# Kernel tuning notes

Hardware: AMD Instinct MI355X
Metric: run time of the kernel (lower is better)

## Reference

```python
import jax, jax.numpy as jnp
import numpy as np

BN_EPS = 1e-5


def setup_inputs() -> dict:
    key = jax.random.key(0)
    ks = jax.random.split(key, 6)
    B, C, H, W = 4, 256, 64, 64
    Ci = 128
    s_in = 0.02  # small init scale for conv weights
    x = jax.random.normal(ks[0], (B, C, H, W), dtype=jnp.float32)
    g_w = jax.random.normal(ks[1], (Ci, C), dtype=jnp.float32) * s_in
    theta_w = jax.random.normal(ks[2], (Ci, C), dtype=jnp.float32) * s_in
    phi_w = jax.random.normal(ks[3], (Ci, C), dtype=jnp.float32) * s_in
    W_w = jax.random.normal(ks[4], (C, Ci), dtype=jnp.float32) * s_in
    return {
        "x": x,
        "g_w": g_w, "g_b": jnp.zeros((Ci,), jnp.float32),
        "theta_w": theta_w, "theta_b": jnp.zeros((Ci,), jnp.float32),
        "phi_w": phi_w, "phi_b": jnp.zeros((Ci,), jnp.float32),
        "W_w": W_w, "W_b": jnp.zeros((C,), jnp.float32),
        "bn_gamma": jnp.ones((C,), jnp.float32),
        "bn_beta": jnp.zeros((C,), jnp.float32),
    }


def reference(x, g_w, g_b, theta_w, theta_b, phi_w, phi_b, W_w, W_b, bn_gamma, bn_beta):
    B, C, H, W = x.shape
    N = H * W
    xf = x.reshape(B, C, N)  # flatten spatial -> [B, C, N]

    def conv1x1(w, b):  # 1x1 conv == per-position linear over channels
        return jnp.einsum('oc,bcn->bon', w, xf) + b[None, :, None]

    g_x = conv1x1(g_w, g_b)          # [B, Ci, N]
    theta_x = conv1x1(theta_w, theta_b)
    phi_x = conv1x1(phi_w, phi_b)

    f = jnp.einsum('bcn,bcm->bnm', theta_x, phi_x)   # [B, N, N] attention logits
    attn = jax.nn.softmax(f, axis=-1)
    y = jnp.einsum('bnm,bcm->bcn', attn, g_x)        # [B, Ci, N]

    Wy = jnp.einsum('oc,bcn->bon', W_w, y) + W_b[None, :, None]  # [B, C, N]
    Wy = Wy.reshape(B, C, H, W)

    # BatchNorm2d in training mode (default): batch statistics over (B, H, W)
    mean = Wy.mean(axis=(0, 2, 3))
    var = Wy.var(axis=(0, 2, 3))
    Wy_bn = (bn_gamma[None, :, None, None] * (Wy - mean[None, :, None, None])
             * jax.lax.rsqrt(var[None, :, None, None] + BN_EPS)
             + bn_beta[None, :, None, None])
    return Wy_bn + x
```

## Files before the change

kernel.cpp:

```cpp
#include <hip/hip_runtime.h>
#include <hip/hip_bf16.h>

typedef __attribute__((ext_vector_type(8))) __bf16 bf16x8;
typedef __attribute__((ext_vector_type(4))) __bf16 bf16x4;
typedef __attribute__((ext_vector_type(4))) float  f32x4;
typedef __attribute__((ext_vector_type(16))) float f32x16;

#define L2E 1.44269504088896340736f

static __device__ __forceinline__ f32x4 mfma16(bf16x8 a, bf16x8 b, f32x4 c) {
    return __builtin_amdgcn_mfma_f32_16x16x32_bf16(a, b, c, 0, 0, 0);
}
static __device__ __forceinline__ f32x16 mfma32(bf16x8 a, bf16x8 b, f32x16 c) {
    return __builtin_amdgcn_mfma_f32_32x32x16_bf16(a, b, c, 0, 0, 0);
}

#define GLOAD_LDS16(gsrc, ldst)                                                \
    __builtin_amdgcn_global_load_lds(                                          \
        (const __attribute__((address_space(1))) unsigned int*)(gsrc),         \
        (__attribute__((address_space(3))) unsigned int*)(ldst), 16, 0, 0)

__global__ __launch_bounds__(256) void prep_w(
    const float* __restrict__ thw, const float* __restrict__ phw,
    const float* __restrict__ gw,  const float* __restrict__ Ww,
    __bf16* __restrict__ wbf)
{
    const int idx  = blockIdx.x * 256 + threadIdx.x;
    const int base = idx * 4;
    const float* src = (base < 32768) ? thw : (base < 65536) ? phw
                     : (base < 98304) ? gw  : Ww;
    const int off = base & 32767;
    f32x4 v = *reinterpret_cast<const f32x4*>(src + off);
    bf16x4 o;
    #pragma unroll
    for (int i = 0; i < 4; ++i) o[i] = (__bf16)v[i];
    *reinterpret_cast<bf16x4*>(wbf + base) = o;
}

__global__ __launch_bounds__(256) void xT_kernel(
    const float* __restrict__ x, __bf16* __restrict__ xT)
{
    __shared__ float tile[64][65];
    const int b  = blockIdx.z;
    const int c0 = blockIdx.y * 64;
    const int n0 = blockIdx.x * 64;
    const int tr = threadIdx.x >> 4;
    const int tc = threadIdx.x & 15;
    #pragma unroll
    for (int k = 0; k < 4; ++k) {
        int c = k * 16 + tr;
        f32x4 v = *reinterpret_cast<const f32x4*>(
            x + ((size_t)b * 256 + c0 + c) * 4096 + n0 + tc * 4);
        #pragma unroll
        for (int i = 0; i < 4; ++i) tile[c][tc * 4 + i] = v[i];
    }
    __syncthreads();
    #pragma unroll
    for (int k = 0; k < 4; ++k) {
        int n = k * 16 + tr;
        bf16x4 v;
        #pragma unroll
        for (int i = 0; i < 4; ++i) v[i] = (__bf16)tile[tc * 4 + i][n];
        *reinterpret_cast<bf16x4*>(xT + ((size_t)b * 4096 + n0 + n) * 256 + c0 + tc * 4) = v;
    }
}

__global__ __launch_bounds__(256, 1) void proj_mfma(
    const __bf16* __restrict__ xT, const __bf16* __restrict__ wbf,
    const float* __restrict__ bth, const float* __restrict__ bph,
    const float* __restrict__ bg,
    __bf16* __restrict__ thetaT, __bf16* __restrict__ phiT, __bf16* __restrict__ gBlk)
{
    const int p    = blockIdx.y;
    const int b    = blockIdx.z;
    const int n0   = blockIdx.x * 64;
    const int w    = threadIdx.x >> 6;
    const int lane = threadIdx.x & 63;
    const int lo   = lane & 15;
    const int hi   = lane >> 4;

    __shared__ alignas(16) __bf16 XA[64 * 256];
    __shared__ alignas(16) __bf16 WL[128 * 256];

    const __bf16* wsrc  = wbf + p * 32768;
    const float*  bias  = (p == 0) ? bth : (p == 1) ? bph : bg;
    const __bf16* xbase = xT + ((size_t)b * 4096 + n0) * 256;

    #pragma unroll
    for (int u = 0; u < 8; ++u) {
        const int chunk = (w * 8 + u) * 64 + lane;
        const int row   = chunk >> 5;
        const int jb    = (chunk & 31) * 16;
        const int sb    = row * 512 + (jb ^ ((row & 7) << 4));
        GLOAD_LDS16(xbase + (sb >> 1), &XA[(w * 8 + u) * 512]);
    }
    #pragma unroll
    for (int u = 0; u < 16; ++u) {
        const int chunk = (w * 16 + u) * 64 + lane;
        const int row   = chunk >> 5;
        const int jb    = (chunk & 31) * 16;
        const int sb    = row * 512 + (jb ^ ((row & 7) << 4));
        GLOAD_LDS16(wsrc + (sb >> 1), &WL[(w * 16 + u) * 512]);
    }
    __syncthreads();

    f32x4 C[8];
    #pragma unroll
    for (int cc = 0; cc < 8; ++cc) C[cc] = f32x4{0.f, 0.f, 0.f, 0.f};

    const int arow = w * 16 + lo;
    #pragma unroll
    for (int kb = 0; kb < 8; ++kb) {
        const int koff = kb * 64 + hi * 16;
        bf16x8 a = *reinterpret_cast<const bf16x8*>(
            (const char*)XA + arow * 512 + (koff ^ ((arow & 7) << 4)));
        bf16x8 bb[8];
        #pragma unroll
        for (int cc = 0; cc < 8; ++cc) {
            const int o = cc * 16 + lo;
            bb[cc] = *reinterpret_cast<const bf16x8*>(
                (const char*)WL + o * 512 + (koff ^ ((o & 7) << 4)));
        }
        #pragma unroll
        for (int cc = 0; cc < 8; ++cc) C[cc] = mfma16(a, bb[cc], C[cc]);
    }

    if (p < 2) {
        __bf16* out = (p == 0) ? thetaT : phiT;
        const int nbase = n0 + w * 16;
        #pragma unroll
        for (int cc = 0; cc < 8; ++cc) {
            const float bv = bias[cc * 16 + lo];
            #pragma unroll
            for (int r = 0; r < 4; ++r)
                out[((size_t)b * 4096 + nbase + 4 * hi + r) * 128 + cc * 16 + lo] =
                    (__bf16)(C[cc][r] + bv);
        }
    } else {
        __syncthreads();
        __bf16* T = &XA[0];
        const int nl0 = w * 16 + 4 * hi;
        #pragma unroll
        for (int cc = 0; cc < 8; ++cc) {
            const float bv = bias[cc * 16 + lo];
            #pragma unroll
            for (int r = 0; r < 4; ++r)
                T[(cc * 16 + lo) * 66 + nl0 + r] = (__bf16)(C[cc][r] + bv);
        }
        __syncthreads();
        #pragma unroll
        for (int q8 = 0; q8 < 8; ++q8) {
            const int qid = q8 * 256 + threadIdx.x;
            const int c   = qid >> 4;
            const int nl  = (qid & 15) * 4;
            const int n   = n0 + nl;
            const int mt  = n >> 5;
            const int mm  = n & 31;
            const int g   = mm >> 2;
            const int gp  = (g & 4) | ((g & 1) << 1) | ((g >> 1) & 1);
            bf16x4 v;
            #pragma unroll
            for (int i = 0; i < 4; ++i) v[i] = T[c * 66 + nl + i];
            *reinterpret_cast<bf16x4*>(
                gBlk + (((size_t)(b * 128 + mt)) * 128 + c) * 32 + (gp << 2)) = v;
        }
    }
}

template<int NCH>
__global__ __launch_bounds__(256, 3) void attn_kernel(
    const __bf16* __restrict__ thetaT, const __bf16* __restrict__ phiT,
    const __bf16* __restrict__ gBlk, __bf16* __restrict__ yPart,
    float* __restrict__ lPart)
{
    constexpr int SH = (NCH == 8) ? 3 : 2;
    constexpr int NT = (4096 / NCH) / 32;
    const int bid   = blockIdx.x;
    const int chunk = bid & (NCH - 1);
    const int qb    = (bid >> SH) & 31;
    const int b     = bid >> (SH + 5);
    const int w     = threadIdx.x >> 6;
    const int lane  = threadIdx.x & 63;
    const int l31   = lane & 31;
    const int h2    = lane >> 5;
    const int Q0    = qb * 128 + w * 32;
    const int kvbase = chunk * (4096 / NCH);

    __shared__ alignas(16) __bf16 Kt[3][32 * 128];
    __shared__ alignas(16) __bf16 Vt[3][128 * 32];

    bf16x8 qf[8];
    {
        const __bf16* qrow = thetaT + ((size_t)b * 4096 + Q0 + l31) * 128 + h2 * 8;
        #pragma unroll
        for (int ks = 0; ks < 8; ++ks)
            qf[ks] = *reinterpret_cast<const bf16x8*>(qrow + ks * 16);
    }

    f32x16 yacc[4];
    #pragma unroll
    for (int ct = 0; ct < 4; ++ct)
        #pragma unroll
        for (int r = 0; r < 16; ++r) yacc[ct][r] = 0.f;
    float ylrun = 0.f;

    const __bf16* phiB   = phiT + (size_t)b * 4096 * 128;
    const __bf16* gBlk_b = gBlk + (size_t)b * 128 * 4096;

    auto stage = [&](int buf, int t) {
        const int kv = kvbase + t * 32;
        #pragma unroll
        for (int u = 0; u < 2; ++u) {
            const int ii   = w + u * 4;
            const int mrow = ii * 4 + (lane >> 4);
            const int cbl  = ((lane & 15) * 16) ^ ((mrow & 7) << 4);
            const __bf16* src = phiB + ((size_t)(kv + mrow) << 7) + (cbl >> 1);
            GLOAD_LDS16(src, &Kt[buf][ii * 512]);
        }
        const __bf16* vtile = gBlk_b + ((size_t)(kv >> 5) << 12);
        #pragma unroll
        for (int u = 0; u < 2; ++u) {
            const int jj = w + u * 4;
            const int ch = jj * 64 + lane;
            const int c  = ch >> 2;
            const int h  = (ch & 3) ^ ((c >> 1) & 3);
            const __bf16* src = vtile + c * 32 + h * 8;
            GLOAD_LDS16(src, &Vt[buf][jj * 512]);
        }
    };

    stage(0, 0);
    stage(1, 1);

    int ia = 0, ib = 1, ic = 2;
    const int sw = (l31 >> 1) & 3;

    #pragma unroll 1
    for (int t = 0; t < NT; ++t) {
        if (t < NT - 2) {
            stage(ic, t + 2);
            asm volatile("s_waitcnt vmcnt(8)" ::: "memory");
        } else if (t == NT - 2) {
            asm volatile("s_waitcnt vmcnt(4)" ::: "memory");
        } else {
            asm volatile("s_waitcnt vmcnt(0)" ::: "memory");
        }
        __builtin_amdgcn_s_barrier();
        __builtin_amdgcn_sched_barrier(0);

        const char* Kb = (const char*)&Kt[ia][0];
        const char* Vb = (const char*)&Vt[ia][0];

        f32x16 S;
        #pragma unroll
        for (int r = 0; r < 16; ++r) S[r] = 0.f;
        #pragma unroll
        for (int ks = 0; ks < 8; ++ks) {
            bf16x8 ka = *reinterpret_cast<const bf16x8*>(
                Kb + l31 * 256 + ((ks * 32 + h2 * 16) ^ ((l31 & 7) << 4)));
            S = mfma32(ka, qf[ks], S);
        }

        float p[16];
        #pragma unroll
        for (int r = 0; r < 16; ++r) p[r] = __builtin_amdgcn_exp2f(S[r] * L2E);
        float ls = 0.f;
        #pragma unroll
        for (int r = 0; r < 16; ++r) ls += p[r];
        ylrun += ls;
        bf16x8 pa0, pa1;
        #pragma unroll
        for (int e = 0; e < 8; ++e) { pa0[e] = (__bf16)p[e]; pa1[e] = (__bf16)p[8 + e]; }

        #pragma unroll
        for (int ct = 0; ct < 4; ++ct) {
            const int vrow = (ct * 32 + l31) * 64;
            bf16x8 v0 = *reinterpret_cast<const bf16x8*>(Vb + vrow + ((h2 ^ sw) << 4));
            bf16x8 v1 = *reinterpret_cast<const bf16x8*>(Vb + vrow + (((2 + h2) ^ sw) << 4));
            yacc[ct] = mfma32(pa0, v0, yacc[ct]);
            yacc[ct] = mfma32(pa1, v1, yacc[ct]);
        }

        asm volatile("" ::: "memory");
        __builtin_amdgcn_s_barrier();
        __builtin_amdgcn_sched_barrier(0);
        const int tmp = ia; ia = ib; ib = ic; ic = tmp;
    }

    const float ylt = ylrun + __shfl_xor(ylrun, 32);
    const int bc = chunk * 4 + b;
    #pragma unroll
    for (int ct = 0; ct < 4; ++ct)
        #pragma unroll
        for (int r = 0; r < 16; ++r) {
            const int q = Q0 + (r & 3) + 8 * (r >> 2) + 4 * h2;
            yPart[((size_t)bc * 4096 + q) * 128 + ct * 32 + l31] = (__bf16)yacc[ct][r];
        }
    if (h2 == 0)
        lPart[(size_t)bc * 4096 + Q0 + l31] = ylt;
}

template<int NC>
__global__ __launch_bounds__(256) void linv_kernel(
    const float* __restrict__ lPart, float* __restrict__ linv)
{
    const int i = blockIdx.x * 256 + threadIdx.x;
    float s = 0.f;
    #pragma unroll
    for (int c = 0; c < NC; ++c) s += lPart[(size_t)c * 16384 + i];
    linv[i] = 1.0f / s;
}

template<int NC>
__global__ __launch_bounds__(256, 1) void wy_mfma(
    const __bf16* __restrict__ yPart, const float* __restrict__ linv,
    const __bf16* __restrict__ wW, const float* __restrict__ Wb,
    __bf16* __restrict__ Wy, float* __restrict__ pSQ)
{
    const int b    = blockIdx.y;
    const int n0   = blockIdx.x * 64;
    const int w    = threadIdx.x >> 6;
    const int lane = threadIdx.x & 63;
    const int lo   = lane & 15;
    const int hi   = lane >> 4;

    __shared__ alignas(16) __bf16 YL[64 * 128];
    __shared__ alignas(16) __bf16 WL[256 * 128];

    #pragma unroll
    for (int u = 0; u < 16; ++u) {
        const int chunk = (w * 16 + u) * 64 + lane;
        const int row   = chunk >> 4;
        const int jb    = (chunk & 15) * 16;
        const int sb    = row * 256 + (jb ^ ((row & 7) << 4));
        GLOAD_LDS16(wW + (sb >> 1), &WL[(w * 16 + u) * 512]);
    }
    #pragma unroll
    for (int u = 0; u < 4; ++u) {
        const int ch   = u * 256 + threadIdx.x;
        const int row  = ch >> 4;
        const int col8 = ch & 15;
        float acc8[8];
        #pragma unroll
        for (int e = 0; e < 8; ++e) acc8[e] = 0.f;
        #pragma unroll
        for (int c = 0; c < NC; ++c) {
            bf16x8 v = *reinterpret_cast<const bf16x8*>(
                yPart + ((size_t)(c * 4 + b) * 4096 + n0 + row) * 128 + col8 * 8);
            #pragma unroll
            for (int e = 0; e < 8; ++e) acc8[e] += (float)v[e];
        }
        bf16x8 o8;
        #pragma unroll
        for (int e = 0; e < 8; ++e) o8[e] = (__bf16)acc8[e];
        *reinterpret_cast<bf16x8*>(
            (char*)YL + row * 256 + ((col8 * 16) ^ ((row & 7) << 4))) = o8;
    }
    __syncthreads();

    f32x4 C[4][4];
    #pragma unroll
    for (int og = 0; og < 4; ++og)
        #pragma unroll
        for (int ct = 0; ct < 4; ++ct) C[og][ct] = f32x4{0.f, 0.f, 0.f, 0.f};

    #pragma unroll
    for (int kb = 0; kb < 4; ++kb) {
        const int koff = kb * 64 + hi * 16;
        bf16x8 a[4], bb[4];
        #pragma unroll
        for (int og = 0; og < 4; ++og) {
            const int o = w * 64 + og * 16 + lo;
            a[og] = *reinterpret_cast<const bf16x8*>(
                (const char*)WL + o * 256 + (koff ^ ((o & 7) << 4)));
        }
        #pragma unroll
        for (int ct = 0; ct < 4; ++ct) {
            const int nl = ct * 16 + lo;
            bb[ct] = *reinterpret_cast<const bf16x8*>(
                (const char*)YL + nl * 256 + (koff ^ ((nl & 7) << 4)));
        }
        #pragma unroll
        for (int og = 0; og < 4; ++og)
            #pragma unroll
            for (int ct = 0; ct < 4; ++ct)
                C[og][ct] = mfma16(a[og], bb[ct], C[og][ct]);
    }

    float linvv[4];
    #pragma unroll
    for (int ct = 0; ct < 4; ++ct)
        linvv[ct] = linv[b * 4096 + n0 + ct * 16 + lo];

    const int blk = blockIdx.y * 64 + blockIdx.x;
    #pragma unroll
    for (int og = 0; og < 4; ++og)
        #pragma unroll
        for (int r = 0; r < 4; ++r) {
            const int o  = w * 64 + og * 16 + 4 * hi + r;
            const float bv = Wb[o];
            float s = 0.f, q = 0.f;
            #pragma unroll
            for (int ct = 0; ct < 4; ++ct) {
                const float v = C[og][ct][r] * linvv[ct] + bv;
                Wy[((size_t)b * 256 + o) * 4096 + n0 + ct * 16 + lo] = (__bf16)v;
                s += v; q += v * v;
            }
            #pragma unroll
            for (int off = 1; off <= 8; off <<= 1) {
                s += __shfl_xor(s, off);
                q += __shfl_xor(q, off);
            }
            if (lo == 0) {
                pSQ[blk * 256 + o]         = s;
                pSQ[65536 + blk * 256 + o] = q;
            }
        }
}

__global__ __launch_bounds__(256) void stats_finalize(
    const float* __restrict__ pSQ, const float* __restrict__ gamma,
    const float* __restrict__ beta, float* __restrict__ stats)
{
    const int o = blockIdx.x;
    const int t = threadIdx.x;
    float s = pSQ[t * 256 + o];
    float q = pSQ[65536 + t * 256 + o];
    #pragma unroll
    for (int off = 32; off >= 1; off >>= 1) {
        s += __shfl_down(s, off);
        q += __shfl_down(q, off);
    }
    __shared__ float red[8];
    const int wid = t >> 6;
    if ((t & 63) == 0) { red[wid] = s; red[4 + wid] = q; }
    __syncthreads();
    if (t == 0) {
        const float S = red[0] + red[1] + red[2] + red[3];
        const float Q = red[4] + red[5] + red[6] + red[7];
        const float mean = S * (1.f / 16384.f);
        const float var  = Q * (1.f / 16384.f) - mean * mean;
        const float scl  = gamma[o] * rsqrtf(var + 1e-5f);
        stats[o]       = scl;
        stats[256 + o] = beta[o] - mean * scl;
    }
}

__global__ __launch_bounds__(256) void final_kernel(
    const __bf16* __restrict__ Wy, const float* __restrict__ x,
    const float* __restrict__ stats, float* __restrict__ out)
{
    const int idx = blockIdx.x * 256 + threadIdx.x;
    const int o   = (idx >> 10) & 255;
    bf16x4 wyb = *reinterpret_cast<const bf16x4*>(Wy + (size_t)idx * 4);
    f32x4 xv = *reinterpret_cast<const f32x4*>(x + (size_t)idx * 4);
    const float scl = stats[o], sh = stats[256 + o];
    f32x4 res;
    #pragma unroll
    for (int i = 0; i < 4; ++i) res[i] = (float)wyb[i] * scl + sh + xv[i];
    *reinterpret_cast<f32x4*>(out + (size_t)idx * 4) = res;
}

extern "C" void kernel_launch(void* const* d_in, const int* in_sizes, int n_in,
                              void* d_out, int out_size, void* d_ws, size_t ws_size,
                              hipStream_t stream)
{
    const float* x    = (const float*)d_in[0];
    const float* g_w  = (const float*)d_in[1];
    const float* g_b  = (const float*)d_in[2];
    const float* th_w = (const float*)d_in[3];
    const float* th_b = (const float*)d_in[4];
    const float* ph_w = (const float*)d_in[5];
    const float* ph_b = (const float*)d_in[6];
    const float* W_w  = (const float*)d_in[7];
    const float* W_b  = (const float*)d_in[8];
    const float* bn_g = (const float*)d_in[9];
    const float* bn_b = (const float*)d_in[10];
    float* out = (float*)d_out;

    char* ws = (char*)d_ws;
    const size_t MB = 1u << 20;
    __bf16* thetaT = (__bf16*)(ws);
    __bf16* phiT   = (__bf16*)(ws + 4 * MB);
    __bf16* gBlk   = (__bf16*)(ws + 8 * MB);
    __bf16* xT     = (__bf16*)(ws + 12 * MB);
    __bf16* yPart  = (__bf16*)(ws + 12 * MB);
    __bf16* Wy     = (__bf16*)(ws);
    float*  pSQ    = (float*) (ws + 8 * MB);
    float*  linv   = (float*) (ws + 8 * MB + 524288);

    const bool big = ws_size >= 46926848ull;
    const size_t tail = big ? 44 * MB : 28 * MB;
    float*  lPart = (float*) (ws + tail);
    __bf16* wbf   = (__bf16*)(ws + tail + (big ? 524288 : 262144));
    float*  stats = (float*) (ws + tail + (big ? 786432 : 524288));

    prep_w<<<dim3(128), 256, 0, stream>>>(th_w, ph_w, g_w, W_w, wbf);
    xT_kernel<<<dim3(64, 4, 4), 256, 0, stream>>>(x, xT);
    proj_mfma<<<dim3(64, 3, 4), 256, 0, stream>>>(
        xT, wbf, th_b, ph_b, g_b, thetaT, phiT, gBlk);
    if (big) {
        attn_kernel<8><<<dim3(1024), 256, 0, stream>>>(thetaT, phiT, gBlk, yPart, lPart);
        linv_kernel<8><<<dim3(64), 256, 0, stream>>>(lPart, linv);
        wy_mfma<8><<<dim3(64, 4), 256, 0, stream>>>(yPart, linv, wbf + 98304, W_b, Wy, pSQ);
    } else {
        attn_kernel<4><<<dim3(512), 256, 0, stream>>>(thetaT, phiT, gBlk, yPart, lPart);
        linv_kernel<4><<<dim3(64), 256, 0, stream>>>(lPart, linv);
        wy_mfma<4><<<dim3(64, 4), 256, 0, stream>>>(yPart, linv, wbf + 98304, W_b, Wy, pSQ);
    }
    stats_finalize<<<dim3(256), 256, 0, stream>>>(pSQ, bn_g, bn_b, stats);
    final_kernel<<<dim3(4096), 256, 0, stream>>>(Wy, x, stats, out);
}
```

Before: 94.24 us.

## Fuse x transpose into projection kernel and compute all three projections per block

```diff
diff --git a/kernel.cpp b/kernel.cpp
--- a/kernel.cpp
+++ b/kernel.cpp
@@ -37,132 +37,123 @@
     *reinterpret_cast<bf16x4*>(wbf + base) = o;
 }
 
-__global__ __launch_bounds__(256) void xT_kernel(
-    const float* __restrict__ x, __bf16* __restrict__ xT)
-{
-    __shared__ float tile[64][65];
-    const int b  = blockIdx.z;
-    const int c0 = blockIdx.y * 64;
-    const int n0 = blockIdx.x * 64;
-    const int tr = threadIdx.x >> 4;
-    const int tc = threadIdx.x & 15;
-    #pragma unroll
-    for (int k = 0; k < 4; ++k) {
-        int c = k * 16 + tr;
-        f32x4 v = *reinterpret_cast<const f32x4*>(
-            x + ((size_t)b * 256 + c0 + c) * 4096 + n0 + tc * 4);
-        #pragma unroll
-        for (int i = 0; i < 4; ++i) tile[c][tc * 4 + i] = v[i];
-    }
-    __syncthreads();
-    #pragma unroll
-    for (int k = 0; k < 4; ++k) {
-        int n = k * 16 + tr;
-        bf16x4 v;
-        #pragma unroll
-        for (int i = 0; i < 4; ++i) v[i] = (__bf16)tile[tc * 4 + i][n];
-        *reinterpret_cast<bf16x4*>(xT + ((size_t)b * 4096 + n0 + n) * 256 + c0 + tc * 4) = v;
-    }
-}
-
-__global__ __launch_bounds__(256, 1) void proj_mfma(
-    const __bf16* __restrict__ xT, const __bf16* __restrict__ wbf,
+__global__ __launch_bounds__(256, 1) void proj_fused(
+    const float* __restrict__ x, const __bf16* __restrict__ wbf,
     const float* __restrict__ bth, const float* __restrict__ bph,
     const float* __restrict__ bg,
     __bf16* __restrict__ thetaT, __bf16* __restrict__ phiT, __bf16* __restrict__ gBlk)
 {
-    const int p    = blockIdx.y;
-    const int b    = blockIdx.z;
+    const int b    = blockIdx.y;
     const int n0   = blockIdx.x * 64;
     const int w    = threadIdx.x >> 6;
     const int lane = threadIdx.x & 63;
     const int lo   = lane & 15;
     const int hi   = lane >> 4;
+    const int tr   = threadIdx.x >> 4;
+    const int tc   = threadIdx.x & 15;
 
     __shared__ alignas(16) __bf16 XA[64 * 256];
     __shared__ alignas(16) __bf16 WL[128 * 256];
-
-    const __bf16* wsrc  = wbf + p * 32768;
-    const float*  bias  = (p == 0) ? bth : (p == 1) ? bph : bg;
-    const __bf16* xbase = xT + ((size_t)b * 4096 + n0) * 256;
-
-    #pragma unroll
-    for (int u = 0; u < 8; ++u) {
-        const int chunk = (w * 8 + u) * 64 + lane;
-        const int row   = chunk >> 5;
-        const int jb    = (chunk & 31) * 16;
-        const int sb    = row * 512 + (jb ^ ((row & 7) << 4));
-        GLOAD_LDS16(xbase + (sb >> 1), &XA[(w * 8 + u) * 512]);
-    }
-    #pragma unroll
-    for (int u = 0; u < 16; ++u) {
-        const int chunk = (w * 16 + u) * 64 + lane;
-        const int row   = chunk >> 5;
-        const int jb    = (chunk & 31) * 16;
-        const int sb    = row * 512 + (jb ^ ((row & 7) << 4));
-        GLOAD_LDS16(wsrc + (sb >> 1), &WL[(w * 16 + u) * 512]);
+    __shared__ float TF[64][65];
+
+    #pragma unroll 1
+    for (int cb = 0; cb < 4; ++cb) {
+        if (cb) __syncthreads();
+        #pragma unroll
+        for (int k = 0; k < 4; ++k) {
+            const int cl = k * 16 + tr;
+            f32x4 v = *reinterpret_cast<const f32x4*>(
+                x + ((size_t)b * 256 + cb * 64 + cl) * 4096 + n0 + tc * 4);
+            #pragma unroll
+            for (int i = 0; i < 4; ++i) TF[cl][tc * 4 + i] = v[i];
+        }
+        __syncthreads();
+        #pragma unroll
+        for (int k = 0; k < 4; ++k) {
+            const int nl = k * 16 + tr;
+            bf16x4 v;
+            #pragma unroll
+            for (int i = 0; i < 4; ++i) v[i] = (__bf16)TF[tc * 4 + i][nl];
+            const int dst = nl * 512 + ((cb * 128 + tc * 8) ^ ((nl & 7) << 4));
+            *reinterpret_cast<bf16x4*>((char*)XA + dst) = v;
+        }
     }
     __syncthreads();
 
-    f32x4 C[8];
-    #pragma unroll
-    for (int cc = 0; cc < 8; ++cc) C[cc] = f32x4{0.f, 0.f, 0.f, 0.f};
-
-    const int arow = w * 16 + lo;
-    #pragma unroll
-    for (int kb = 0; kb < 8; ++kb) {
-        const int koff = kb * 64 + hi * 16;
-        bf16x8 a = *reinterpret_cast<const bf16x8*>(
-            (const char*)XA + arow * 512 + (koff ^ ((arow & 7) << 4)));
-        bf16x8 bb[8];
-        #pragma unroll
-        for (int cc = 0; cc < 8; ++cc) {
-            const int o = cc * 16 + lo;
-            bb[cc] = *reinterpret_cast<const bf16x8*>(
-                (const char*)WL + o * 512 + (koff ^ ((o & 7) << 4)));
-        }
-        #pragma unroll
-        for (int cc = 0; cc < 8; ++cc) C[cc] = mfma16(a, bb[cc], C[cc]);
-    }
-
-    if (p < 2) {
-        __bf16* out = (p == 0) ? thetaT : phiT;
-        const int nbase = n0 + w * 16;
-        #pragma unroll
-        for (int cc = 0; cc < 8; ++cc) {
-            const float bv = bias[cc * 16 + lo];
-            #pragma unroll
-            for (int r = 0; r < 4; ++r)
-                out[((size_t)b * 4096 + nbase + 4 * hi + r) * 128 + cc * 16 + lo] =
-                    (__bf16)(C[cc][r] + bv);
-        }
-    } else {
+    #pragma unroll 1
+    for (int p = 0; p < 3; ++p) {
+        if (p) __syncthreads();
+        #pragma unroll
+        for (int u = 0; u < 16; ++u) {
+            const int chunk = (w * 16 + u) * 64 + lane;
+            const int row   = chunk >> 5;
+            const int jb    = (chunk & 31) * 16;
+            const int sb    = row * 512 + (jb ^ ((row & 7) << 4));
+            GLOAD_LDS16(wbf + p * 32768 + (sb >> 1), &WL[(w * 16 + u) * 512]);
+        }
         __syncthreads();
-        __bf16* T = &XA[0];
-        const int nl0 = w * 16 + 4 * hi;
-        #pragma unroll
-        for (int cc = 0; cc < 8; ++cc) {
-            const float bv = bias[cc * 16 + lo];
-            #pragma unroll
-            for (int r = 0; r < 4; ++r)
-                T[(cc * 16 + lo) * 66 + nl0 + r] = (__bf16)(C[cc][r] + bv);
-        }
-        __syncthreads();
-        #pragma unroll
-        for (int q8 = 0; q8 < 8; ++q8) {
-            const int qid = q8 * 256 + threadIdx.x;
-            const int c   = qid >> 4;
-            const int nl  = (qid & 15) * 4;
-            const int n   = n0 + nl;
-            const int mt  = n >> 5;
-            const int mm  = n & 31;
-            const int g   = mm >> 2;
-            const int gp  = (g & 4) | ((g & 1) << 1) | ((g >> 1) & 1);
-            bf16x4 v;
-            #pragma unroll
-            for (int i = 0; i < 4; ++i) v[i] = T[c * 66 + nl + i];
-            *reinterpret_cast<bf16x4*>(
-                gBlk + (((size_t)(b * 128 + mt)) * 128 + c) * 32 + (gp << 2)) = v;
+
+        f32x4 C[8];
+        #pragma unroll
+        for (int cc = 0; cc < 8; ++cc) C[cc] = f32x4{0.f, 0.f, 0.f, 0.f};
+
+        const int arow = w * 16 + lo;
+        #pragma unroll
+        for (int kb = 0; kb < 8; ++kb) {
+            const int koff = kb * 64 + hi * 16;
+            bf16x8 a = *reinterpret_cast<const bf16x8*>(
+                (const char*)XA + arow * 512 + (koff ^ ((arow & 7) << 4)));
+            bf16x8 bb[8];
+            #pragma unroll
+            for (int cc = 0; cc < 8; ++cc) {
+                const int o = cc * 16 + lo;
+                bb[cc] = *reinterpret_cast<const bf16x8*>(
+                    (const char*)WL + o * 512 + (koff ^ ((o & 7) << 4)));
+            }
+            #pragma unroll
+            for (int cc = 0; cc < 8; ++cc) C[cc] = mfma16(a, bb[cc], C[cc]);
+        }
+
+        const float* bias = (p == 0) ? bth : (p == 1) ? bph : bg;
+        if (p < 2) {
+            __bf16* out = (p == 0) ? thetaT : phiT;
+            const int nbase = n0 + w * 16;
+            #pragma unroll
+            for (int cc = 0; cc < 8; ++cc) {
+                const float bv = bias[cc * 16 + lo];
+                #pragma unroll
+                for (int r = 0; r < 4; ++r)
+                    out[((size_t)b * 4096 + nbase + 4 * hi + r) * 128 + cc * 16 + lo] =
+                        (__bf16)(C[cc][r] + bv);
+            }
+        } else {
+            __syncthreads();
+            __bf16* T = &XA[0];
+            const int nl0 = w * 16 + 4 * hi;
+            #pragma unroll
+            for (int cc = 0; cc < 8; ++cc) {
+                const float bv = bias[cc * 16 + lo];
+                #pragma unroll
+                for (int r = 0; r < 4; ++r)
+                    T[(cc * 16 + lo) * 66 + nl0 + r] = (__bf16)(C[cc][r] + bv);
+            }
+            __syncthreads();
+            #pragma unroll
+            for (int q8 = 0; q8 < 8; ++q8) {
+                const int qid = q8 * 256 + threadIdx.x;
+                const int c   = qid >> 4;
+                const int nl  = (qid & 15) * 4;
+                const int n   = n0 + nl;
+                const int mt  = n >> 5;
+                const int mm  = n & 31;
+                const int g   = mm >> 2;
+                const int gp  = (g & 4) | ((g & 1) << 1) | ((g >> 1) & 1);
+                bf16x4 v;
+                #pragma unroll
+                for (int i = 0; i < 4; ++i) v[i] = T[c * 66 + nl + i];
+                *reinterpret_cast<bf16x4*>(
+                    gBlk + (((size_t)(b * 128 + mt)) * 128 + c) * 32 + (gp << 2)) = v;
+            }
         }
     }
 }
@@ -483,7 +474,6 @@
     __bf16* thetaT = (__bf16*)(ws);
     __bf16* phiT   = (__bf16*)(ws + 4 * MB);
     __bf16* gBlk   = (__bf16*)(ws + 8 * MB);
-    __bf16* xT     = (__bf16*)(ws + 12 * MB);
     __bf16* yPart  = (__bf16*)(ws + 12 * MB);
     __bf16* Wy     = (__bf16*)(ws);
     float*  pSQ    = (float*) (ws + 8 * MB);
@@ -496,9 +486,8 @@
     float*  stats = (float*) (ws + tail + (big ? 786432 : 524288));
 
     prep_w<<<dim3(128), 256, 0, stream>>>(th_w, ph_w, g_w, W_w, wbf);
-    xT_kernel<<<dim3(64, 4, 4), 256, 0, stream>>>(x, xT);
-    proj_mfma<<<dim3(64, 3, 4), 256, 0, stream>>>(
-        xT, wbf, th_b, ph_b, g_b, thetaT, phiT, gBlk);
+    proj_fused<<<dim3(64, 4), 256, 0, stream>>>(
+        x, wbf, th_b, ph_b, g_b, thetaT, phiT, gBlk);
     if (big) {
         attn_kernel<8><<<dim3(1024), 256, 0, stream>>>(thetaT, phiT, gBlk, yPart, lPart);
         linv_kernel<8><<<dim3(64), 256, 0, stream>>>(lPart, linv);
```

Result: faster. 91.03 us (-3.4%).
